# Kernel tuning notes

Measured on AMD Instinct MI355X. Metric: run time of the kernel, lower is better.

The kernel has to match this reference:

```python
import jax, jax.numpy as jnp
import numpy as np
import math

PHI = (1 + math.sqrt(5)) / 2
ALPHA = 1 / PHI          # residual scale
BETA = 1 / PHI ** 2      # sparse-matmul scale
DIM = 1910
NZ = int(DIM * DIM / PHI)


def setup_inputs() -> dict:
    key = jax.random.key(0)
    kx, ki, kv = jax.random.split(key, 3)
    x = jax.random.normal(kx, (8, 4096, DIM), dtype=jnp.float32)
    W_indices = jax.random.randint(ki, (2, NZ), 0, DIM, dtype=jnp.int32)
    W_values = jax.random.normal(kv, (NZ,), dtype=jnp.float32) / math.sqrt(DIM)
    return {"x": x, "W_indices": W_indices, "W_values": W_values}


def reference(x, W_indices, W_values):
    dim = x.shape[-1]
    # COO -> dense: duplicate (row,col) entries sum, matching torch.sparse semantics.
    W = jnp.zeros((dim, dim), dtype=x.dtype).at[W_indices[0], W_indices[1]].add(W_values)
    orig_shape = x.shape
    xf = x.reshape(-1, dim)          # [tokens, dim]
    Wx = xf @ W.T                    # (W @ x.T).T == x @ W.T
    out = ALPHA * xf + BETA * Wx
    return out.reshape(orig_shape)
```

## Files before the change

kernel.cpp:

```cpp
#include <hip/hip_runtime.h>
#include <hip/hip_bf16.h>
#include <stdint.h>

#define DIMV 1910
#define KP   1920
#define NT   30
#define PHI_F  1.6180339887498949f
#define BETA_F 0.3819660112501051f

typedef __attribute__((ext_vector_type(4))) float f32x4;
typedef __attribute__((ext_vector_type(8))) short bf16x8;
typedef __attribute__((ext_vector_type(8))) unsigned short u16x8;

__device__ __forceinline__ void gl16(const void* g, void* l) {
    __builtin_amdgcn_global_load_lds(
        (const __attribute__((address_space(1))) void*)(uintptr_t)g,
        (__attribute__((address_space(3))) void*)(uint32_t)(uintptr_t)l,
        16, 0, 0);
}

__global__ void k_prep(const float* __restrict__ x, unsigned short* __restrict__ xb, int total8,
                       const int* __restrict__ ridx, const int* __restrict__ cidx,
                       const float* __restrict__ vals, float* __restrict__ Wd, int nz) {
    const int tid  = threadIdx.x;
    const int half = (int)gridDim.x >> 1;
    const int b    = (int)blockIdx.x >> 1;
    const int stride = half * 256;
    if ((blockIdx.x & 1) == 0) {
        for (int i = b * 256 + tid; i < total8; i += stride) {
            int v = i * 8;
            int row = v / KP;
            int col = v - row * KP;
            u16x8 o;
            if (col + 8 <= DIMV) {
                const float2* s = (const float2*)(x + (size_t)row * DIMV + col);
                float2 f0 = s[0], f1 = s[1], f2 = s[2], f3 = s[3];
                float f[8] = {f0.x, f0.y, f1.x, f1.y, f2.x, f2.y, f3.x, f3.y};
#pragma unroll
                for (int j = 0; j < 8; ++j) {
                    __hip_bfloat16 bb = __float2bfloat16(f[j]);
                    o[j] = *reinterpret_cast<unsigned short*>(&bb);
                }
            } else {
#pragma unroll
                for (int j = 0; j < 8; ++j) {
                    int c = col + j;
                    float fv = (c < DIMV) ? x[(size_t)row * DIMV + c] : 0.f;
                    __hip_bfloat16 bb = __float2bfloat16(fv);
                    o[j] = *reinterpret_cast<unsigned short*>(&bb);
                }
            }
            *(u16x8*)(xb + (size_t)v) = o;
        }
    } else {
        for (int i = b * 256 + tid; i < nz; i += stride)
            atomicAdd(Wd + (size_t)ridx[i] * DIMV + cidx[i], vals[i]);
    }
}

__global__ void k_build_w(const float* __restrict__ Wd, unsigned short* __restrict__ Wb, int total8) {
    int stride = gridDim.x * blockDim.x;
    for (int i = blockIdx.x * blockDim.x + threadIdx.x; i < total8; i += stride) {
        int v = i * 8;
        int n = v / KP;
        int k = v - n * KP;
        u16x8 o;
#pragma unroll
        for (int j = 0; j < 8; ++j) {
            int kk = k + j;
            float fv = (n < DIMV && kk < DIMV) ? Wd[(size_t)n * DIMV + kk] : 0.f;
            if (kk == n && n < DIMV) fv += PHI_F;
            __hip_bfloat16 b = __float2bfloat16(fv);
            o[j] = *reinterpret_cast<unsigned short*>(&b);
        }
        *(u16x8*)(Wb + (size_t)v) = o;
    }
}

__global__ __launch_bounds__(512, 2) void k_gemm(const short* __restrict__ A,
                                                 const short* __restrict__ B,
                                                 float* __restrict__ C) {
    __shared__ char lds[131072];

    const int bid = blockIdx.x;
    const int bn  = bid & 7;
    const int bmg = bid >> 3;

    const int tid = threadIdx.x;
    const int w   = tid >> 6;
    const int l   = tid & 63;
    const int wm  = w >> 2;
    const int wn  = w & 3;
    const int fr  = l & 15;
    const int q   = l >> 4;

    const int    srow = tid >> 3;
    const size_t KPB  = (size_t)KP * 2;
    const int    swz  = ((tid & 7) ^ (srow & 7)) * 16;
    const char*  aSrc0 = (const char*)A + (size_t)(bmg * 256 + srow) * KPB + swz;
    const char*  bSrc  = (const char*)B + (size_t)(bn * 256 + srow) * KPB + swz;
    char* stDst = lds + tid * 16;

    const int co0  = ((q    ) ^ (fr & 7)) * 16;
    const int co1  = ((4 + q) ^ (fr & 7)) * 16;
    const int aOff = (wm * 128 + fr) * 128;
    const int bOff = 32768 + (wn * 64 + fr) * 128;

    f32x4 acc[8][4] = {};

#define STAGE_A(src, tt, bo, s) gl16((src) + (size_t)(s) * 64 * KPB + (size_t)(tt) * 128, stDst + (bo) + (s) * 8192)
#define STAGE_B(tt, bo, s)      gl16(bSrc  + (size_t)(s) * 64 * KPB + (size_t)(tt) * 128, stDst + (bo) + 32768 + (s) * 8192)

#pragma unroll
    for (int s = 0; s < 4; ++s) STAGE_A(aSrc0, 0, 0, s);
#pragma unroll
    for (int s = 0; s < 4; ++s) STAGE_B(0, 0, s);
    asm volatile("s_waitcnt vmcnt(0)" ::: "memory");
    __builtin_amdgcn_s_barrier();
    asm volatile("" ::: "memory");

    for (int mt = 0; mt < 4; ++mt) {
        const char* aSrc = aSrc0 + (size_t)mt * 8192 * KPB;
        int bo = 0;

        for (int t = 0; t < NT; ++t) {
            const int nbo = bo ^ 65536;
            const char* pa = lds + bo + aOff;
            const char* pb = lds + bo + bOff;
            const bool st  = (mt < 3) || (t + 1 < NT);
            const int  tts = (t + 1 < NT) ? (t + 1) : 0;
            const char* aS = (t + 1 < NT) ? aSrc : aSrc + (size_t)8192 * KPB;
            bf16x8 a[4][2], b[2][2];

#pragma unroll
            for (int mi = 0; mi < 4; ++mi) {
                a[mi][0] = *(const bf16x8*)(pa + mi * 2048 + co0);
                a[mi][1] = *(const bf16x8*)(pa + mi * 2048 + co1);
            }
#pragma unroll
            for (int ni = 0; ni < 2; ++ni) {
                b[ni][0] = *(const bf16x8*)(pb + ni * 2048 + co0);
                b[ni][1] = *(const bf16x8*)(pb + ni * 2048 + co1);
            }
            if (st) { STAGE_A(aS, tts, nbo, 0); STAGE_A(aS, tts, nbo, 1); STAGE_A(aS, tts, nbo, 2); }
            asm volatile("s_waitcnt lgkmcnt(8)" ::: "memory");
            __builtin_amdgcn_s_barrier();
            asm volatile("s_waitcnt lgkmcnt(0)" ::: "memory");
            __builtin_amdgcn_sched_barrier(0);
            __builtin_amdgcn_s_setprio(1);
#pragma unroll
            for (int kk = 0; kk < 2; ++kk)
#pragma unroll
                for (int mi = 0; mi < 4; ++mi)
#pragma unroll
                    for (int ni = 0; ni < 2; ++ni)
                        acc[mi][ni] = __builtin_amdgcn_mfma_f32_16x16x32_bf16(a[mi][kk], b[ni][kk], acc[mi][ni], 0, 0, 0);
            __builtin_amdgcn_s_setprio(0);
            asm volatile("" ::: "memory");
            __builtin_amdgcn_s_barrier();
            asm volatile("" ::: "memory");

#pragma unroll
            for (int ni = 0; ni < 2; ++ni) {
                b[ni][0] = *(const bf16x8*)(pb + 4096 + ni * 2048 + co0);
                b[ni][1] = *(const bf16x8*)(pb + 4096 + ni * 2048 + co1);
            }
            if (st) { STAGE_A(aS, tts, nbo, 3); STAGE_B(tts, nbo, 0); STAGE_B(tts, nbo, 1); }
            asm volatile("" ::: "memory");
            __builtin_amdgcn_s_barrier();
            asm volatile("s_waitcnt lgkmcnt(0)" ::: "memory");
            __builtin_amdgcn_sched_barrier(0);
            __builtin_amdgcn_s_setprio(1);
#pragma unroll
            for (int kk = 0; kk < 2; ++kk)
#pragma unroll
                for (int mi = 0; mi < 4; ++mi)
#pragma unroll
                    for (int ni = 0; ni < 2; ++ni)
                        acc[mi][ni + 2] = __builtin_amdgcn_mfma_f32_16x16x32_bf16(a[mi][kk], b[ni][kk], acc[mi][ni + 2], 0, 0, 0);
            __builtin_amdgcn_s_setprio(0);
            asm volatile("" ::: "memory");
            __builtin_amdgcn_s_barrier();
            asm volatile("" ::: "memory");

#pragma unroll
            for (int mi = 0; mi < 4; ++mi) {
                a[mi][0] = *(const bf16x8*)(pa + 8192 + mi * 2048 + co0);
                a[mi][1] = *(const bf16x8*)(pa + 8192 + mi * 2048 + co1);
            }
            if (st) { STAGE_B(tts, nbo, 2); STAGE_B(tts, nbo, 3); }
            asm volatile("" ::: "memory");
            __builtin_amdgcn_s_barrier();
            asm volatile("s_waitcnt lgkmcnt(0)" ::: "memory");
            __builtin_amdgcn_sched_barrier(0);
            __builtin_amdgcn_s_setprio(1);
#pragma unroll
            for (int kk = 0; kk < 2; ++kk)
#pragma unroll
                for (int mi = 0; mi < 4; ++mi)
#pragma unroll
                    for (int ni = 0; ni < 2; ++ni)
                        acc[mi + 4][ni + 2] = __builtin_amdgcn_mfma_f32_16x16x32_bf16(a[mi][kk], b[ni][kk], acc[mi + 4][ni + 2], 0, 0, 0);
            __builtin_amdgcn_s_setprio(0);
            asm volatile("" ::: "memory");
            __builtin_amdgcn_s_barrier();
            asm volatile("" ::: "memory");

#pragma unroll
            for (int ni = 0; ni < 2; ++ni) {
                b[ni][0] = *(const bf16x8*)(pb + ni * 2048 + co0);
                b[ni][1] = *(const bf16x8*)(pb + ni * 2048 + co1);
            }
            asm volatile("" ::: "memory");
            __builtin_amdgcn_s_barrier();
            asm volatile("s_waitcnt lgkmcnt(0)" ::: "memory");
            __builtin_amdgcn_sched_barrier(0);
            __builtin_amdgcn_s_setprio(1);
#pragma unroll
            for (int kk = 0; kk < 2; ++kk)
#pragma unroll
                for (int mi = 0; mi < 4; ++mi)
#pragma unroll
                    for (int ni = 0; ni < 2; ++ni)
                        acc[mi + 4][ni] = __builtin_amdgcn_mfma_f32_16x16x32_bf16(a[mi][kk], b[ni][kk], acc[mi + 4][ni], 0, 0, 0);
            __builtin_amdgcn_s_setprio(0);
            asm volatile("s_waitcnt vmcnt(0)" ::: "memory");
            __builtin_amdgcn_s_barrier();
            asm volatile("" ::: "memory");

            bo = nbo;
        }

        const int bm    = mt * 32 + bmg;
        const int grow0 = bm * 256 + wm * 128 + q * 4;
        const int gcol0 = bn * 256 + wn * 64 + fr;
#pragma unroll
        for (int ei = 0; ei < 8; ++ei) {
#pragma unroll
            for (int ni = 0; ni < 4; ++ni) {
                int gcol = gcol0 + ni * 16;
                if (gcol < DIMV) {
                    size_t base = (size_t)(grow0 + ei * 16) * DIMV + gcol;
#pragma unroll
                    for (int r = 0; r < 4; ++r)
                        C[base + (size_t)r * DIMV] = BETA_F * acc[ei][ni][r];
                }
            }
        }
        if (mt < 3) {
#pragma unroll
            for (int ei = 0; ei < 8; ++ei)
#pragma unroll
                for (int ni = 0; ni < 4; ++ni)
                    acc[ei][ni] = (f32x4)(0.f);
        }
    }
#undef STAGE_A
#undef STAGE_B
}

extern "C" void kernel_launch(void* const* d_in, const int* in_sizes, int n_in,
                              void* d_out, int out_size, void* d_ws, size_t ws_size,
                              hipStream_t stream) {
    const float* x    = (const float*)d_in[0];
    const int*   widx = (const int*)d_in[1];
    const float* wval = (const float*)d_in[2];
    float* out = (float*)d_out;

    const int nz = in_sizes[2];
    const int M  = in_sizes[0] / DIMV;

    const size_t xb_bytes = (size_t)M * KP * 2;
    const size_t wb_bytes = (size_t)2048 * KP * 2;
    const size_t wd_bytes = (size_t)DIMV * DIMV * 4;
    char* ws = (char*)d_ws;
    unsigned short* xb = (unsigned short*)ws;
    unsigned short* Wb = (unsigned short*)(ws + xb_bytes);
    float*          Wd = (float*)(ws + xb_bytes + wb_bytes);
    if (ws_size < xb_bytes + wb_bytes + wd_bytes) return;

    hipMemsetAsync(Wd, 0, wd_bytes, stream);
    k_prep<<<2048, 256, 0, stream>>>(x, xb, M * KP / 8, widx, widx + nz, wval, Wd, nz);
    k_build_w<<<1800, 256, 0, stream>>>(Wd, Wb, KP * KP / 8);
    k_gemm<<<256, 512, 0, stream>>>((const short*)xb, (const short*)Wb, out);
}
```

Before: 399.2 us.

## Triple-buffer A tiles and flatten M/K loops into one pipelined loop

The nested m-tile/k-tile loops become a single flat loop of 120 steps. A tiles are triple-buffered (prefetched two steps ahead) and B tiles double-buffered, using 160KB of LDS, so the pipeline no longer drains between m-tiles and loads have more time in flight. The block index mapping is swapped so adjacent blocks share the same B column tile, and the last two MFMA phases are merged to drop one barrier. The larger LDS footprint may limit occupancy to one block per CU despite launch_bounds(512,2).

```diff
diff --git a/kernel.cpp b/kernel.cpp
--- a/kernel.cpp
+++ b/kernel.cpp
@@ -5,6 +5,7 @@
 #define DIMV 1910
 #define KP   1920
 #define NT   30
+#define TT   120
 #define PHI_F  1.6180339887498949f
 #define BETA_F 0.3819660112501051f
 
@@ -80,11 +81,11 @@
 __global__ __launch_bounds__(512, 2) void k_gemm(const short* __restrict__ A,
                                                  const short* __restrict__ B,
                                                  float* __restrict__ C) {
-    __shared__ char lds[131072];
+    __shared__ char lds[163840];
 
     const int bid = blockIdx.x;
-    const int bn  = bid & 7;
-    const int bmg = bid >> 3;
+    const int bmg = bid & 31;
+    const int bn  = bid >> 5;
 
     const int tid = threadIdx.x;
     const int w   = tid >> 6;
@@ -97,163 +98,164 @@
     const int    srow = tid >> 3;
     const size_t KPB  = (size_t)KP * 2;
     const int    swz  = ((tid & 7) ^ (srow & 7)) * 16;
-    const char*  aSrc0 = (const char*)A + (size_t)(bmg * 256 + srow) * KPB + swz;
-    const char*  bSrc  = (const char*)B + (size_t)(bn * 256 + srow) * KPB + swz;
+    const char*  bSrc = (const char*)B + (size_t)(bn * 256 + srow) * KPB + swz;
+    const size_t sweep = (size_t)64 * KPB;
     char* stDst = lds + tid * 16;
 
     const int co0  = ((q    ) ^ (fr & 7)) * 16;
     const int co1  = ((4 + q) ^ (fr & 7)) * 16;
     const int aOff = (wm * 128 + fr) * 128;
-    const int bOff = 32768 + (wn * 64 + fr) * 128;
+    const int bOff = (wn * 64 + fr) * 128;
 
     f32x4 acc[8][4] = {};
 
-#define STAGE_A(src, tt, bo, s) gl16((src) + (size_t)(s) * 64 * KPB + (size_t)(tt) * 128, stDst + (bo) + (s) * 8192)
-#define STAGE_B(tt, bo, s)      gl16(bSrc  + (size_t)(s) * 64 * KPB + (size_t)(tt) * 128, stDst + (bo) + 32768 + (s) * 8192)
+#define STAGE_A(src, kk_, dstoff, s) gl16((src) + (size_t)(s) * sweep + (size_t)(kk_) * 128, stDst + (dstoff) + (s) * 8192)
+#define STAGE_B(kk_, dstoff, s)      gl16(bSrc  + (size_t)(s) * sweep + (size_t)(kk_) * 128, stDst + 98304 + (dstoff) + (s) * 8192)
+
+    const char* aSrc0 = (const char*)A + (size_t)(bmg * 256 + srow) * KPB + swz;
+    const size_t mstep = (size_t)8192 * KPB;
 
 #pragma unroll
     for (int s = 0; s < 4; ++s) STAGE_A(aSrc0, 0, 0, s);
 #pragma unroll
     for (int s = 0; s < 4; ++s) STAGE_B(0, 0, s);
-    asm volatile("s_waitcnt vmcnt(0)" ::: "memory");
+#pragma unroll
+    for (int s = 0; s < 4; ++s) STAGE_A(aSrc0, 1, 32768, s);
+    asm volatile("s_waitcnt vmcnt(4)" ::: "memory");
     __builtin_amdgcn_s_barrier();
     asm volatile("" ::: "memory");
 
-    for (int mt = 0; mt < 4; ++mt) {
-        const char* aSrc = aSrc0 + (size_t)mt * 8192 * KPB;
-        int bo = 0;
-
-        for (int t = 0; t < NT; ++t) {
-            const int nbo = bo ^ 65536;
-            const char* pa = lds + bo + aOff;
-            const char* pb = lds + bo + bOff;
-            const bool st  = (mt < 3) || (t + 1 < NT);
-            const int  tts = (t + 1 < NT) ? (t + 1) : 0;
-            const char* aS = (t + 1 < NT) ? aSrc : aSrc + (size_t)8192 * KPB;
-            bf16x8 a[4][2], b[2][2];
-
-#pragma unroll
-            for (int mi = 0; mi < 4; ++mi) {
-                a[mi][0] = *(const bf16x8*)(pa + mi * 2048 + co0);
-                a[mi][1] = *(const bf16x8*)(pa + mi * 2048 + co1);
-            }
-#pragma unroll
-            for (int ni = 0; ni < 2; ++ni) {
-                b[ni][0] = *(const bf16x8*)(pb + ni * 2048 + co0);
-                b[ni][1] = *(const bf16x8*)(pb + ni * 2048 + co1);
-            }
-            if (st) { STAGE_A(aS, tts, nbo, 0); STAGE_A(aS, tts, nbo, 1); STAGE_A(aS, tts, nbo, 2); }
-            asm volatile("s_waitcnt lgkmcnt(8)" ::: "memory");
-            __builtin_amdgcn_s_barrier();
-            asm volatile("s_waitcnt lgkmcnt(0)" ::: "memory");
-            __builtin_amdgcn_sched_barrier(0);
-            __builtin_amdgcn_s_setprio(1);
-#pragma unroll
-            for (int kk = 0; kk < 2; ++kk)
-#pragma unroll
-                for (int mi = 0; mi < 4; ++mi)
-#pragma unroll
-                    for (int ni = 0; ni < 2; ++ni)
-                        acc[mi][ni] = __builtin_amdgcn_mfma_f32_16x16x32_bf16(a[mi][kk], b[ni][kk], acc[mi][ni], 0, 0, 0);
-            __builtin_amdgcn_s_setprio(0);
-            asm volatile("" ::: "memory");
-            __builtin_amdgcn_s_barrier();
-            asm volatile("" ::: "memory");
-
-#pragma unroll
-            for (int ni = 0; ni < 2; ++ni) {
-                b[ni][0] = *(const bf16x8*)(pb + 4096 + ni * 2048 + co0);
-                b[ni][1] = *(const bf16x8*)(pb + 4096 + ni * 2048 + co1);
-            }
-            if (st) { STAGE_A(aS, tts, nbo, 3); STAGE_B(tts, nbo, 0); STAGE_B(tts, nbo, 1); }
-            asm volatile("" ::: "memory");
-            __builtin_amdgcn_s_barrier();
-            asm volatile("s_waitcnt lgkmcnt(0)" ::: "memory");
-            __builtin_amdgcn_sched_barrier(0);
-            __builtin_amdgcn_s_setprio(1);
-#pragma unroll
-            for (int kk = 0; kk < 2; ++kk)
-#pragma unroll
-                for (int mi = 0; mi < 4; ++mi)
-#pragma unroll
-                    for (int ni = 0; ni < 2; ++ni)
-                        acc[mi][ni + 2] = __builtin_amdgcn_mfma_f32_16x16x32_bf16(a[mi][kk], b[ni][kk], acc[mi][ni + 2], 0, 0, 0);
-            __builtin_amdgcn_s_setprio(0);
-            asm volatile("" ::: "memory");
-            __builtin_amdgcn_s_barrier();
-            asm volatile("" ::: "memory");
-
-#pragma unroll
-            for (int mi = 0; mi < 4; ++mi) {
-                a[mi][0] = *(const bf16x8*)(pa + 8192 + mi * 2048 + co0);
-                a[mi][1] = *(const bf16x8*)(pa + 8192 + mi * 2048 + co1);
-            }
-            if (st) { STAGE_B(tts, nbo, 2); STAGE_B(tts, nbo, 3); }
-            asm volatile("" ::: "memory");
-            __builtin_amdgcn_s_barrier();
-            asm volatile("s_waitcnt lgkmcnt(0)" ::: "memory");
-            __builtin_amdgcn_sched_barrier(0);
-            __builtin_amdgcn_s_setprio(1);
-#pragma unroll
-            for (int kk = 0; kk < 2; ++kk)
-#pragma unroll
-                for (int mi = 0; mi < 4; ++mi)
-#pragma unroll
-                    for (int ni = 0; ni < 2; ++ni)
-                        acc[mi + 4][ni + 2] = __builtin_amdgcn_mfma_f32_16x16x32_bf16(a[mi][kk], b[ni][kk], acc[mi + 4][ni + 2], 0, 0, 0);
-            __builtin_amdgcn_s_setprio(0);
-            asm volatile("" ::: "memory");
-            __builtin_amdgcn_s_barrier();
-            asm volatile("" ::: "memory");
-
-#pragma unroll
-            for (int ni = 0; ni < 2; ++ni) {
-                b[ni][0] = *(const bf16x8*)(pb + ni * 2048 + co0);
-                b[ni][1] = *(const bf16x8*)(pb + ni * 2048 + co1);
-            }
-            asm volatile("" ::: "memory");
-            __builtin_amdgcn_s_barrier();
-            asm volatile("s_waitcnt lgkmcnt(0)" ::: "memory");
-            __builtin_amdgcn_sched_barrier(0);
-            __builtin_amdgcn_s_setprio(1);
-#pragma unroll
-            for (int kk = 0; kk < 2; ++kk)
-#pragma unroll
-                for (int mi = 0; mi < 4; ++mi)
-#pragma unroll
-                    for (int ni = 0; ni < 2; ++ni)
-                        acc[mi + 4][ni] = __builtin_amdgcn_mfma_f32_16x16x32_bf16(a[mi][kk], b[ni][kk], acc[mi + 4][ni], 0, 0, 0);
-            __builtin_amdgcn_s_setprio(0);
-            asm volatile("s_waitcnt vmcnt(0)" ::: "memory");
-            __builtin_amdgcn_s_barrier();
-            asm volatile("" ::: "memory");
-
-            bo = nbo;
-        }
-
-        const int bm    = mt * 32 + bmg;
-        const int grow0 = bm * 256 + wm * 128 + q * 4;
-        const int gcol0 = bn * 256 + wn * 64 + fr;
-#pragma unroll
-        for (int ei = 0; ei < 8; ++ei) {
-#pragma unroll
-            for (int ni = 0; ni < 4; ++ni) {
-                int gcol = gcol0 + ni * 16;
-                if (gcol < DIMV) {
-                    size_t base = (size_t)(grow0 + ei * 16) * DIMV + gcol;
-#pragma unroll
-                    for (int r = 0; r < 4; ++r)
-                        C[base + (size_t)r * DIMV] = BETA_F * acc[ei][ni][r];
+    int boA = 0, stA = 65536;
+    int boB = 0, stB = 32768;
+    int tkR = 0;
+    int kb1 = 1;
+    int ka2 = 2;
+    int mtR = 0;
+    const char* aStage = aSrc0;
+
+    for (int t = 0; t < TT; ++t) {
+        const char* pa = lds + boA + aOff;
+        const char* pb = lds + 98304 + boB + bOff;
+        const bool stb = (t + 1 < TT);
+        const bool sta = (t + 2 < TT);
+        bf16x8 a[4][2], b0[2][2], b1[2][2];
+
+#pragma unroll
+        for (int mi = 0; mi < 4; ++mi) {
+            a[mi][0] = *(const bf16x8*)(pa + mi * 2048 + co0);
+            a[mi][1] = *(const bf16x8*)(pa + mi * 2048 + co1);
+        }
+#pragma unroll
+        for (int ni = 0; ni < 2; ++ni) {
+            b0[ni][0] = *(const bf16x8*)(pb + ni * 2048 + co0);
+            b0[ni][1] = *(const bf16x8*)(pb + ni * 2048 + co1);
+        }
+        if (stb) { STAGE_B(kb1, stB, 0); STAGE_B(kb1, stB, 1); }
+        asm volatile("s_waitcnt lgkmcnt(8)" ::: "memory");
+        __builtin_amdgcn_s_barrier();
+        asm volatile("s_waitcnt lgkmcnt(0)" ::: "memory");
+        __builtin_amdgcn_sched_barrier(0);
+        __builtin_amdgcn_s_setprio(1);
+#pragma unroll
+        for (int kk = 0; kk < 2; ++kk)
+#pragma unroll
+            for (int mi = 0; mi < 4; ++mi)
+#pragma unroll
+                for (int ni = 0; ni < 2; ++ni)
+                    acc[mi][ni] = __builtin_amdgcn_mfma_f32_16x16x32_bf16(a[mi][kk], b0[ni][kk], acc[mi][ni], 0, 0, 0);
+        __builtin_amdgcn_s_setprio(0);
+        asm volatile("" ::: "memory");
+        __builtin_amdgcn_s_barrier();
+        asm volatile("" ::: "memory");
+
+#pragma unroll
+        for (int ni = 0; ni < 2; ++ni) {
+            b1[ni][0] = *(const bf16x8*)(pb + 4096 + ni * 2048 + co0);
+            b1[ni][1] = *(const bf16x8*)(pb + 4096 + ni * 2048 + co1);
+        }
+        if (stb) { STAGE_B(kb1, stB, 2); STAGE_B(kb1, stB, 3); }
+        if (sta) { STAGE_A(aStage, ka2, stA, 0); STAGE_A(aStage, ka2, stA, 1); }
+        asm volatile("" ::: "memory");
+        __builtin_amdgcn_s_barrier();
+        asm volatile("s_waitcnt lgkmcnt(0)" ::: "memory");
+        __builtin_amdgcn_sched_barrier(0);
+        __builtin_amdgcn_s_setprio(1);
+#pragma unroll
+        for (int kk = 0; kk < 2; ++kk)
+#pragma unroll
+            for (int mi = 0; mi < 4; ++mi)
+#pragma unroll
+                for (int ni = 0; ni < 2; ++ni)
+                    acc[mi][ni + 2] = __builtin_amdgcn_mfma_f32_16x16x32_bf16(a[mi][kk], b1[ni][kk], acc[mi][ni + 2], 0, 0, 0);
+        __builtin_amdgcn_s_setprio(0);
+        asm volatile("" ::: "memory");
+        __builtin_amdgcn_s_barrier();
+        asm volatile("" ::: "memory");
+
+#pragma unroll
+        for (int mi = 0; mi < 4; ++mi) {
+            a[mi][0] = *(const bf16x8*)(pa + 8192 + mi * 2048 + co0);
+            a[mi][1] = *(const bf16x8*)(pa + 8192 + mi * 2048 + co1);
+        }
+        if (sta) { STAGE_A(aStage, ka2, stA, 2); STAGE_A(aStage, ka2, stA, 3); }
+        asm volatile("" ::: "memory");
+        __builtin_amdgcn_s_barrier();
+        asm volatile("s_waitcnt lgkmcnt(0)" ::: "memory");
+        __builtin_amdgcn_sched_barrier(0);
+        __builtin_amdgcn_s_setprio(1);
+#pragma unroll
+        for (int kk = 0; kk < 2; ++kk)
+#pragma unroll
+            for (int mi = 0; mi < 4; ++mi)
+#pragma unroll
+                for (int ni = 0; ni < 2; ++ni)
+                    acc[mi + 4][ni + 2] = __builtin_amdgcn_mfma_f32_16x16x32_bf16(a[mi][kk], b1[ni][kk], acc[mi + 4][ni + 2], 0, 0, 0);
+#pragma unroll
+        for (int kk = 0; kk < 2; ++kk)
+#pragma unroll
+            for (int mi = 0; mi < 4; ++mi)
+#pragma unroll
+                for (int ni = 0; ni < 2; ++ni)
+                    acc[mi + 4][ni] = __builtin_amdgcn_mfma_f32_16x16x32_bf16(a[mi][kk], b0[ni][kk], acc[mi + 4][ni], 0, 0, 0);
+        __builtin_amdgcn_s_setprio(0);
+        if (sta) { asm volatile("s_waitcnt vmcnt(4)" ::: "memory"); }
+        else     { asm volatile("s_waitcnt vmcnt(0)" ::: "memory"); }
+        __builtin_amdgcn_s_barrier();
+        asm volatile("" ::: "memory");
+
+        if (tkR == NT - 1) {
+            const int bm    = mtR * 32 + bmg;
+            const int grow0 = bm * 256 + wm * 128 + q * 4;
+            const int gcol0 = bn * 256 + wn * 64 + fr;
+#pragma unroll
+            for (int ei = 0; ei < 8; ++ei) {
+#pragma unroll
+                for (int ni = 0; ni < 4; ++ni) {
+                    int gcol = gcol0 + ni * 16;
+                    if (gcol < DIMV) {
+                        size_t base = (size_t)(grow0 + ei * 16) * DIMV + gcol;
+#pragma unroll
+                        for (int r = 0; r < 4; ++r)
+                            C[base + (size_t)r * DIMV] = BETA_F * acc[ei][ni][r];
+                    }
                 }
             }
-        }
-        if (mt < 3) {
-#pragma unroll
-            for (int ei = 0; ei < 8; ++ei)
-#pragma unroll
-                for (int ni = 0; ni < 4; ++ni)
-                    acc[ei][ni] = (f32x4)(0.f);
-        }
+            if (t + 1 < TT) {
+#pragma unroll
+                for (int ei = 0; ei < 8; ++ei)
+#pragma unroll
+                    for (int ni = 0; ni < 4; ++ni)
+                        acc[ei][ni] = (f32x4)(0.f);
+            }
+            tkR = 0; ++mtR;
+        } else ++tkR;
+
+        boA = (boA == 65536) ? 0 : boA + 32768;
+        stA = (stA == 65536) ? 0 : stA + 32768;
+        boB ^= 32768;
+        stB ^= 32768;
+        if (++kb1 == NT) kb1 = 0;
+        if (++ka2 == NT) { ka2 = 0; aStage += mstep; }
     }
 #undef STAGE_A
 #undef STAGE_B
```

After: 390.2 us. 2.3% less time.
